# Kernel tuning notes

Measured on AMD Instinct MI355X. Metric: run time of the kernel, lower is better.

## Reference

```python
import jax, jax.numpy as jnp
import numpy as np

B = 4096
HIST = 50
VOCAB = 100000
PAD_IDX = 179
EMB_DIM = 64           # sparse_dim_after_embedding
DENSE = 256            # dense_feature_number
PROJ_IN = 768          # emb_feature_dim_before_project
PROJ_HID = 256
PROJ_OUT = 64          # emb_feature_dim
BOT = (512, 64)        # bottom_mlp_dims
ALL_DIM = EMB_DIM + BOT[1] + PROJ_OUT        # 192
OUT_DIM = ALL_DIM * (ALL_DIM + 1) // 2 + BOT[1]  # 18592
TOP = (1024, 512)      # top_mlp_dims
BN_EPS = 1e-5

# precomputed upper-triangular (incl. diagonal) indices, row-major like torch mask extract
_TRIU_R, _TRIU_C = np.triu_indices(ALL_DIM)


def setup_inputs() -> dict:
    key = jax.random.key(0)
    ks = jax.random.split(key, 20)
    s = 0.02
    emb_table = jax.random.normal(ks[0], (VOCAB, EMB_DIM), jnp.float32) * s
    emb_table = emb_table.at[PAD_IDX].set(0.0)  # padding_idx=179
    return {
        "x_sparse": jax.random.randint(ks[1], (B, HIST), 0, VOCAB),
        "x_dense": jax.random.normal(ks[2], (B, DENSE), jnp.float32),
        "x_embed_before_projection": jax.random.normal(ks[3], (B, PROJ_IN), jnp.float32),
        "emb_table": emb_table,
        "pw1": jax.random.normal(ks[4], (PROJ_IN, PROJ_HID), jnp.float32) * s,
        "pb1": jnp.zeros((PROJ_HID,), jnp.float32),
        "pw2": jax.random.normal(ks[5], (PROJ_HID, PROJ_OUT), jnp.float32) * s,
        "pb2": jnp.zeros((PROJ_OUT,), jnp.float32),
        "bn_gamma": jnp.ones((PROJ_OUT,), jnp.float32),
        "bn_beta": jnp.zeros((PROJ_OUT,), jnp.float32),
        "bw1": jax.random.normal(ks[6], (DENSE, BOT[0]), jnp.float32) * s,
        "bb1": jnp.zeros((BOT[0],), jnp.float32),
        "bw2": jax.random.normal(ks[7], (BOT[0], BOT[1]), jnp.float32) * s,
        "bb2": jnp.zeros((BOT[1],), jnp.float32),
        "tw1": jax.random.normal(ks[8], (OUT_DIM, TOP[0]), jnp.float32) * s,
        "tb1": jnp.zeros((TOP[0],), jnp.float32),
        "tw2": jax.random.normal(ks[9], (TOP[0], TOP[1]), jnp.float32) * s,
        "tb2": jnp.zeros((TOP[1],), jnp.float32),
        "tw3": jax.random.normal(ks[10], (TOP[1], 1), jnp.float32) * s,
        "tb3": jnp.zeros((1,), jnp.float32),
    }


def reference(x_sparse, x_dense, x_embed_before_projection, emb_table,
              pw1, pb1, pw2, pb2, bn_gamma, bn_beta,
              bw1, bb1, bw2, bb2, tw1, tb1, tw2, tb2, tw3, tb3):
    # embedding-sum over history: [B, HIST, EMB_DIM] -> [B, EMB_DIM]
    embed_x = jnp.sum(emb_table[x_sparse], axis=1)

    # ContrastiveNet: Linear -> ReLU -> Linear -> BatchNorm1d (batch stats, training fwd)
    h = jax.nn.relu(x_embed_before_projection @ pw1 + pb1)
    z = h @ pw2 + pb2
    mu = jnp.mean(z, axis=0)
    var = jnp.var(z, axis=0)  # biased variance, as torch BN uses for normalization
    x_embed = bn_gamma * (z - mu) * jax.lax.rsqrt(var + BN_EPS) + bn_beta

    # bottom MLP (dropout = identity at inference)
    bottom = jax.nn.relu(jax.nn.relu(x_dense @ bw1 + bb1) @ bw2 + bb2)

    concat_first = jnp.concatenate([bottom, x_embed, embed_x], axis=-1)  # [B, 192]

    # pairwise dot-product interaction; pack upper triangle incl. diagonal
    dot = jnp.einsum('bi,bj->bij', concat_first, concat_first)  # [B, 192, 192]
    interaction = dot[:, _TRIU_R, _TRIU_C]  # [B, 192*193/2]

    concat_second = jnp.concatenate([interaction, bottom], axis=-1)  # [B, OUT_DIM]

    t = jax.nn.relu(concat_second @ tw1 + tb1)
    t = jax.nn.relu(t @ tw2 + tb2)
    output = jax.nn.sigmoid(t @ tw3 + tb3)  # [B, 1]
    # squeeze(-1).squeeze().unsqueeze(1) -> [B, 1]
    output = output.reshape(-1, 1)
    return output, x_embed
```

## Files before the change

### kernel.cpp

```cpp
#include <hip/hip_runtime.h>
#include <hip/hip_bf16.h>
#include <cstdint>
#include <cstddef>

typedef __bf16 bf16;
typedef unsigned char u8;
typedef unsigned short u16;
typedef __bf16 v8bf  __attribute__((ext_vector_type(8)));
typedef float  f32x4 __attribute__((ext_vector_type(4)));
typedef float  f32x16 __attribute__((ext_vector_type(16)));
typedef int    i32x4 __attribute__((ext_vector_type(4)));
typedef int    i32x2 __attribute__((ext_vector_type(2)));
typedef int    v8i32 __attribute__((ext_vector_type(8)));

__device__ __forceinline__ void async16(void* lds, const void* g) {
  __builtin_amdgcn_global_load_lds(
      (const __attribute__((address_space(1))) unsigned int*)g,
      (__attribute__((address_space(3))) unsigned int*)lds, 16, 0, 0);
}


__device__ __forceinline__ void pairs_dev(u16* __restrict__ pairs, float* __restrict__ stats) {
  int r = threadIdx.x;
  if (r < 128) stats[r] = 0.f;
  if (r < 192) {
    int off = 192 * r - (r * (r - 1)) / 2;
    for (int c = r; c < 192; ++c) pairs[off + c - r] = (u16)((r << 8) | c);
  } else if (r == 192) {
    for (int j = 0; j < 64; ++j) pairs[18528 + j] = (u16)((j << 8) | 192);
  } else if (r == 193) {
    for (int j = 18592; j < 18624; ++j) pairs[j] = (u16)((192 << 8) | 192);
  }
}

__device__ __forceinline__ void packA_dev(const float* __restrict__ A,
                                          bf16* __restrict__ Ap, int K,
                                          int bx, int by) {
  const int t = threadIdx.x;
  const int KT = K >> 5;
  const size_t tile = ((size_t)bx * KT + by) * (64 * 32);
  const int c = t;
  const int mm = c >> 2, koct = (c & 3) * 8;
  const float* src = A + (size_t)(bx * 64 + mm) * K + by * 32 + koct;
  f32x4 f0 = *(const f32x4*)src;
  f32x4 f1 = *(const f32x4*)(src + 4);
  __align__(16) bf16 h[8];
  h[0]=(bf16)f0[0]; h[1]=(bf16)f0[1]; h[2]=(bf16)f0[2]; h[3]=(bf16)f0[3];
  h[4]=(bf16)f1[0]; h[5]=(bf16)f1[1]; h[6]=(bf16)f1[2]; h[7]=(bf16)f1[3];
  *(i32x4*)(Ap + tile + (size_t)c * 8) = *(const i32x4*)h;
}

__device__ __forceinline__ void packB_dev(const float* __restrict__ B,
                                          bf16* __restrict__ Bp, int K, int N,
                                          int bx, int by,
                                          float* __restrict__ sLB) {
  const int BNp = 64, LS = 66;
  const int t = threadIdx.x;
  const int KT = K >> 5;
  for (int idx = t; idx < 32 * BNp; idx += 256) {
    const int kk = idx >> 6, nn = idx & 63;
    sLB[kk * LS + nn] = B[(size_t)(by * 32 + kk) * N + bx * BNp + nn];
  }
  __syncthreads();
  const size_t tile = ((size_t)bx * KT + by) * ((size_t)BNp * 32);
  for (int c = t; c < BNp * 4; c += 256) {
    const int nn = c >> 2, koct = (c & 3) * 8;
    __align__(16) bf16 h[8];
#pragma unroll
    for (int j = 0; j < 8; ++j) h[j] = (bf16)sLB[(koct + j) * LS + nn];
    *(i32x4*)(Bp + tile + (size_t)c * 8) = *(const i32x4*)h;
  }
}

__device__ __forceinline__ void packTw1_dev(const float* __restrict__ tw1,
                                            u8* __restrict__ Bp, int nt, int kw) {
  const int t = threadIdx.x;
  const int n4 = t & 31, k8 = t >> 5;
  const int kbase = kw * 64 + k8 * 8;
  const int nbase = nt * 128 + n4 * 4;
  f32x4 v[8];
#pragma unroll
  for (int j = 0; j < 8; ++j) {
    const int gk = kbase + j;
    if (gk < 18592) {
      v[j] = *(const f32x4*)(tw1 + (size_t)gk * 1024 + nbase);
      v[j] *= 32.f;
    } else {
      v[j] = f32x4{0.f, 0.f, 0.f, 0.f};
    }
  }
  u8* tile = Bp + ((size_t)nt * 291 + kw) * 8192;
#pragma unroll
  for (int c = 0; c < 4; ++c) {
    int r0 = __builtin_amdgcn_cvt_pk_fp8_f32(v[0][c], v[1][c], 0, false);
    r0 = __builtin_amdgcn_cvt_pk_fp8_f32(v[2][c], v[3][c], r0, true);
    int r1 = __builtin_amdgcn_cvt_pk_fp8_f32(v[4][c], v[5][c], 0, false);
    r1 = __builtin_amdgcn_cvt_pk_fp8_f32(v[6][c], v[7][c], r1, true);
    i32x2 d; d[0] = r0; d[1] = r1;
    *(i32x2*)(tile + (n4 * 4 + c) * 64 + k8 * 8) = d;
  }
}

__global__ __launch_bounds__(256) void prologue_kernel(
    const float* __restrict__ xep, const float* __restrict__ xd,
    const float* __restrict__ pw1, const float* __restrict__ pw2,
    const float* __restrict__ bw1, const float* __restrict__ bw2,
    const float* __restrict__ tw1, const float* __restrict__ tw2,
    bf16* Xp, bf16* Xd, bf16* Bpw1, bf16* Bpw2, bf16* Bbw1, bf16* Bbw2,
    u8* Btw1, bf16* Btw2, u16* pairs, float* stats) {
  __shared__ float sLB[32 * 66];
  int i = blockIdx.x;
  if (i < 2328) { packTw1_dev(tw1, Btw1, i & 7, i >> 3); return; }
  i -= 2328;
  if (i < 1536) { packA_dev(xep, Xp, 768, i & 63, i >> 6); return; }
  i -= 1536;
  if (i < 512)  { packA_dev(xd, Xd, 256, i & 63, i >> 6); return; }
  i -= 512;
  if (i < 96)   { packB_dev(pw1, Bpw1, 768, 256, i & 3, i >> 2, sLB); return; }
  i -= 96;
  if (i < 8)    { packB_dev(pw2, Bpw2, 256, 64, 0, i, sLB); return; }
  i -= 8;
  if (i < 64)   { packB_dev(bw1, Bbw1, 256, 512, i & 7, i >> 3, sLB); return; }
  i -= 64;
  if (i < 16)   { packB_dev(bw2, Bbw2, 512, 64, 0, i, sLB); return; }
  i -= 16;
  if (i < 256)  { packB_dev(tw2, Btw2, 1024, 512, i & 7, i >> 3, sLB); return; }
  i -= 256;
  if (i == 0) pairs_dev(pairs, stats);
}

__device__ __forceinline__ void embed8_dev(const int* __restrict__ xs,
                                           const float* __restrict__ emb,
                                           float* __restrict__ cf, int blk) {
  const int wid = threadIdx.x >> 6, lane = threadIdx.x & 63;
#pragma unroll
  for (int s = 0; s < 2; ++s) {
    const int b = blk * 8 + s * 4 + wid;
    const int* row = xs + (size_t)b * 50;
    float acc = 0.f;
#pragma unroll 10
    for (int h = 0; h < 50; ++h) {
      int idx = row[h];
      acc += emb[(size_t)idx * 64 + lane];
    }
    cf[(size_t)b * 193 + 128 + lane] = acc;
  }
}

template <int BM, int BN, int MF, int NF>
__device__ __forceinline__ void gemm_body(
    const bf16* __restrict__ Ap, const bf16* __restrict__ Bp,
    const float* __restrict__ bias,
    float* __restrict__ outF, int ldF,
    bf16* __restrict__ outP, int ktN, int bmsh,
    int KT, int M0, int relu_flag, int bx, int by,
    bf16* sA, bf16* sB, float* statsAcc) {
  const int t = threadIdx.x;
  const int wid = t >> 6, lane = t & 63;
  const int wm = (wid >> 1) * (MF * 16);
  const int wn = (wid & 1) * (NF * 16);
  const int r16 = lane & 15, q = lane >> 4;

  f32x4 acc[MF][NF];
#pragma unroll
  for (int i = 0; i < MF; ++i)
#pragma unroll
    for (int j = 0; j < NF; ++j) acc[i][j] = f32x4{0.f, 0.f, 0.f, 0.f};

  const bf16* aBase = Ap + (size_t)bx * KT * (BM * 32);
  const bf16* bBase = Bp + (size_t)by * KT * (BN * 32);
  constexpr int A_CH = BM * 4;
  constexpr int B_CH = BN * 4;

  for (int kt = 0; kt < KT; ++kt) {
    const bf16* ag = aBase + (size_t)kt * (BM * 32);
    const bf16* bg = bBase + (size_t)kt * (BN * 32);
#pragma unroll
    for (int c = t; c < A_CH; c += 256) {
      const int row = c >> 2, qs = c & 3, qg = (qs - (row >> 1)) & 3;
      async16(sA + c * 8, ag + row * 32 + qg * 8);
    }
#pragma unroll
    for (int c = t; c < B_CH; c += 256) {
      const int row = c >> 2, qs = c & 3, qg = (qs - (row >> 1)) & 3;
      async16(sB + c * 8, bg + row * 32 + qg * 8);
    }
    __syncthreads();
    v8bf af[MF], bfr[NF];
#pragma unroll
    for (int i = 0; i < MF; ++i) {
      const int row = wm + i * 16 + r16;
      af[i] = *(const v8bf*)(sA + row * 32 + (((q + (row >> 1)) & 3) * 8));
    }
#pragma unroll
    for (int j = 0; j < NF; ++j) {
      const int row = wn + j * 16 + r16;
      bfr[j] = *(const v8bf*)(sB + row * 32 + (((q + (row >> 1)) & 3) * 8));
    }
#pragma unroll
    for (int i = 0; i < MF; ++i)
#pragma unroll
      for (int j = 0; j < NF; ++j)
        acc[i][j] = __builtin_amdgcn_mfma_f32_16x16x32_bf16(af[i], bfr[j], acc[i][j], 0, 0, 0);
    __syncthreads();
  }

  float cs[NF], cs2[NF];
#pragma unroll
  for (int j = 0; j < NF; ++j) { cs[j] = 0.f; cs2[j] = 0.f; }

#pragma unroll
  for (int j = 0; j < NF; ++j) {
    const int gn = by * BN + wn + j * 16 + r16;
    const float bv = bias[gn];
#pragma unroll
    for (int i = 0; i < MF; ++i) {
      const int gm0 = M0 + bx * BM + wm + i * 16 + q * 4;
#pragma unroll
      for (int r = 0; r < 4; ++r) {
        float v = acc[i][j][r] + bv;
        if (relu_flag) v = fmaxf(v, 0.f);
        if (statsAcc) { cs[j] += v; cs2[j] += v * v; }
        const int gm = gm0 + r;
        if (outF) outF[(size_t)gm * ldF + gn] = v;
        if (outP) {
          const int mt = gm >> bmsh, mm = gm & ((1 << bmsh) - 1);
          outP[(((size_t)mt * ktN + (gn >> 5)) << (bmsh + 5)) + ((size_t)mm << 5) + (gn & 31)] = (bf16)v;
        }
      }
    }
  }

  if (statsAcc) {
#pragma unroll
    for (int j = 0; j < NF; ++j) {
      float a = cs[j], b2 = cs2[j];
      a += __shfl_xor(a, 16, 64);  a += __shfl_xor(a, 32, 64);
      b2 += __shfl_xor(b2, 16, 64); b2 += __shfl_xor(b2, 32, 64);
      if (q == 0) {
        const int gn = by * BN + wn + j * 16 + r16;
        atomicAdd(&statsAcc[gn], a);
        atomicAdd(&statsAcc[64 + gn], b2);
      }
    }
  }
}

template <int BM, int BN, int MF, int NF>
__global__ __launch_bounds__(256, 2) void gemm_kernel(
    const bf16* __restrict__ Ap, const bf16* __restrict__ Bp,
    const float* __restrict__ bias,
    float* __restrict__ outF, int ldF,
    bf16* __restrict__ outP, int ktN, int bmsh,
    int KT, int M0, int relu_flag) {
  __shared__ __align__(16) bf16 sA[BM * 32];
  __shared__ __align__(16) bf16 sB[BN * 32];
  gemm_body<BM, BN, MF, NF>(Ap, Bp, bias, outF, ldF, outP, ktN, bmsh,
                            KT, M0, relu_flag, blockIdx.x, blockIdx.y, sA, sB, nullptr);
}

template <int BM, int BN, int MF, int NF>
__global__ __launch_bounds__(256, 2) void gemm_dual_kernel(
    const bf16* Ap0, const bf16* Bp0, const float* bias0,
    float* outF0, int ldF0, bf16* outP0, int ktN0, int bmsh0, int KT0, int relu0, int gy0,
    float* statsAcc0,
    const bf16* Ap1, const bf16* Bp1, const float* bias1,
    float* outF1, int ldF1, bf16* outP1, int ktN1, int bmsh1, int KT1, int relu1, int gy1,
    const int* xs, const float* emb, float* cf) {
  __shared__ __align__(16) bf16 sA[BM * 32];
  __shared__ __align__(16) bf16 sB[BN * 32];
  if (blockIdx.z == 0) {
    if ((int)blockIdx.y >= gy0) return;
    gemm_body<BM, BN, MF, NF>(Ap0, Bp0, bias0, outF0, ldF0, outP0, ktN0, bmsh0,
                              KT0, 0, relu0, blockIdx.x, blockIdx.y, sA, sB, statsAcc0);
  } else if (blockIdx.z == 1) {
    if ((int)blockIdx.y >= gy1) return;
    gemm_body<BM, BN, MF, NF>(Ap1, Bp1, bias1, outF1, ldF1, outP1, ktN1, bmsh1,
                              KT1, 0, relu1, blockIdx.x, blockIdx.y, sA, sB, nullptr);
  } else {
    embed8_dev(xs, emb, cf, blockIdx.y * 64 + blockIdx.x);
  }
}

template <int S>
__global__ __launch_bounds__(256, 4) void gemm_splitk_mx(
    const u8* __restrict__ Ap, const u8* __restrict__ Bp,
    bf16* __restrict__ part, int Mchunk) {
  __shared__ __align__(16) u8 sAB[4][8192];
  const int t = threadIdx.x;
  const int bx = blockIdx.x, by = blockIdx.y, bz = blockIdx.z;
  const int lane = t & 63, wid = t >> 6;
  const int wm = (wid >> 1) * 64, wn = (wid & 1) * 64;
  const int l31 = lane & 31, khalf = lane >> 5;
  const int kw0 = (291 * bz) / S, kw1 = (291 * (bz + 1)) / S;

  const int r1 = t >> 2;
  const int g1 = r1 * 64 + ((((t & 3) - (r1 >> 1)) & 3) << 4);
  const int r2 = (t + 256) >> 2;
  const int g2 = r2 * 64 + (((((t + 256) & 3) - (r2 >> 1)) & 3) << 4);
  u8* lA = &sAB[0][0] + t * 16;
  u8* lB = &sAB[2][0] + t * 16;

  const u8* fa0[2]; const u8* fa1[2]; const u8* fb0[2]; const u8* fb1[2];
#pragma unroll
  for (int i = 0; i < 2; ++i) {
    const int ra = wm + i * 32 + l31;
    const int qa = (khalf * 2 + (ra >> 1)) & 3;
    fa0[i] = &sAB[0][0] + ra * 64 + qa * 16;
    fa1[i] = &sAB[0][0] + ra * 64 + (((qa + 1) & 3) << 4);
    const int rb = wn + i * 32 + l31;
    const int qb = (khalf * 2 + (rb >> 1)) & 3;
    fb0[i] = &sAB[2][0] + rb * 64 + qb * 16;
    fb1[i] = &sAB[2][0] + rb * 64 + (((qb + 1) & 3) << 4);
  }

  f32x16 acc[2][2];
#pragma unroll
  for (int i = 0; i < 2; ++i)
#pragma unroll
    for (int j = 0; j < 2; ++j)
#pragma unroll
      for (int r = 0; r < 16; ++r) acc[i][j][r] = 0.f;

  const u8* agp = Ap + ((size_t)bx * 291 + kw0) * 8192;
  const u8* bgp = Bp + ((size_t)by * 291 + kw0) * 8192;

  auto compute = [&](int off) {
    v8i32 av[2], bv[2];
#pragma unroll
    for (int i = 0; i < 2; ++i) {
      union { i32x4 h[2]; v8i32 v; } ua;
      ua.h[0] = *(const i32x4*)(fa0[i] + off);
      ua.h[1] = *(const i32x4*)(fa1[i] + off);
      av[i] = ua.v;
      union { i32x4 h[2]; v8i32 v; } ub;
      ub.h[0] = *(const i32x4*)(fb0[i] + off);
      ub.h[1] = *(const i32x4*)(fb1[i] + off);
      bv[i] = ub.v;
    }
#pragma unroll
    for (int i = 0; i < 2; ++i)
#pragma unroll
      for (int j = 0; j < 2; ++j)
        acc[i][j] = __builtin_amdgcn_mfma_scale_f32_32x32x64_f8f6f4(
            av[i], bv[j], acc[i][j], 0, 0,
            0, 0x7F7F7F7F,
            0, 0x7A7A7A7A);
  };

  const int nw = kw1 - kw0;

  async16(lA, agp + g1);  async16(lA + 4096, agp + g2);
  async16(lB, bgp + g1);  async16(lB + 4096, bgp + g2);

  for (int w = 0; w < nw; ++w) {
    const int cur = (w & 1) * 8192;
    const int nxt = 8192 - cur;
    if (w + 1 < nw) {
      const u8* ag = agp + (size_t)(w + 1) * 8192;
      const u8* bg = bgp + (size_t)(w + 1) * 8192;
      async16(lA + nxt, ag + g1);  async16(lA + nxt + 4096, ag + g2);
      async16(lB + nxt, bg + g1);  async16(lB + nxt + 4096, bg + g2);
      asm volatile("s_waitcnt vmcnt(4)" ::: "memory");
    } else {
      asm volatile("s_waitcnt vmcnt(0)" ::: "memory");
    }
    __builtin_amdgcn_s_barrier();
    __builtin_amdgcn_sched_barrier(0);
    __builtin_amdgcn_s_setprio(1);
    compute(cur);
    __builtin_amdgcn_s_setprio(0);
    __builtin_amdgcn_s_barrier();
  }

  bf16* pBase = part + (size_t)bz * Mchunk * 1024;
#pragma unroll
  for (int i = 0; i < 2; ++i)
#pragma unroll
    for (int j = 0; j < 2; ++j) {
      const int gn = by * 128 + wn + j * 32 + l31;
#pragma unroll
      for (int r = 0; r < 16; ++r) {
        const int gm = bx * 128 + wm + i * 32 + (r & 3) + 8 * (r >> 2) + 4 * khalf;
        pBase[(size_t)gm * 1024 + gn] = (bf16)acc[i][j][r];
      }
    }
}

__global__ __launch_bounds__(256) void reducek_kernel(const bf16* __restrict__ part,
                                                      const float* __restrict__ bias,
                                                      bf16* __restrict__ t1,
                                                      int S, int Mchunk, int M0) {
  const int idx = blockIdx.x * 256 + threadIdx.x;
  const int gm = idx >> 7;
  const int gn8 = (idx & 127) * 8;
  float v[8] = {0.f, 0.f, 0.f, 0.f, 0.f, 0.f, 0.f, 0.f};
  for (int s = 0; s < S; ++s) {
    v8bf p = *(const v8bf*)(part + ((size_t)s * Mchunk + gm) * 1024 + gn8);
#pragma unroll
    for (int r = 0; r < 8; ++r) v[r] += (float)p[r];
  }
  const f32x4 b0 = *(const f32x4*)(bias + gn8);
  const f32x4 b1 = *(const f32x4*)(bias + gn8 + 4);
  __align__(16) bf16 h[8];
#pragma unroll
  for (int r = 0; r < 4; ++r) h[r] = (bf16)fmaxf(v[r] + b0[r], 0.f);
#pragma unroll
  for (int r = 0; r < 4; ++r) h[4 + r] = (bf16)fmaxf(v[4 + r] + b1[r], 0.f);
  const int G = M0 + gm;
  const int mt = G >> 6, mm = G & 63, kt = gn8 >> 5;
  *(i32x4*)(t1 + (((size_t)mt * 32 + kt) << 11) + (mm << 5) + (gn8 & 31)) = *(const i32x4*)h;
}

__global__ __launch_bounds__(256, 2) void agen_kernel(const float* __restrict__ cf,
                                                      const float* __restrict__ z,
                                                      const float* __restrict__ gsum,
                                                      const float* __restrict__ gamma,
                                                      const float* __restrict__ beta,
                                                      const u16* __restrict__ pairs,
                                                      u8* __restrict__ Ap,
                                                      float* __restrict__ dout,
                                                      int rowBase) {
  __shared__ float sCF[64 * 193];
  __shared__ float sMu[64], sRstd[64];
  const int t = threadIdx.x;
  const int gRow0 = rowBase + blockIdx.x * 64;
  for (int idx = t; idx < 64 * 64; idx += 256) {
    const int r = idx >> 6, c = idx & 63;
    sCF[r * 193 + c] = cf[(size_t)(gRow0 + r) * 193 + c];
  }
  for (int idx = t; idx < 64 * 64; idx += 256) {
    const int r = idx >> 6, c = idx & 63;
    sCF[r * 193 + 128 + c] = cf[(size_t)(gRow0 + r) * 193 + 128 + c];
  }
  if (t < 64) {
    const float mu = gsum[t] * (1.f / 4096.f);
    const float var = gsum[64 + t] * (1.f / 4096.f) - mu * mu;
    sMu[t] = mu;
    sRstd[t] = rsqrtf(var + 1e-5f);
    sCF[t * 193 + 192] = 1.f;
  }
  __syncthreads();
  for (int idx = t; idx < 64 * 64; idx += 256) {
    const int r = idx >> 6, c = idx & 63;
    const float xe = gamma[c] * (z[(size_t)(gRow0 + r) * 64 + c] - sMu[c]) * sRstd[c] + beta[c];
    sCF[r * 193 + 64 + c] = xe;
    if (blockIdx.y == 0) dout[4096 + (size_t)(gRow0 + r) * 64 + c] = xe;
  }
  __syncthreads();

  const int kw0 = (291 * blockIdx.y) / 8;
  const int kw1 = (291 * (blockIdx.y + 1)) / 8;
  const int row = t >> 2, kq = t & 3;
  const int mt = blockIdx.x >> 1;
  const int mrow = (blockIdx.x & 1) * 64 + row;
  const float* myrow = sCF + row * 193;
  for (int kw = kw0; kw < kw1; ++kw) {
    const int kb = kw * 64 + kq * 16;
    i32x4 d;
    if (kb >= 18592) {
      d = i32x4{0, 0, 0, 0};
    } else {
      union { i32x4 v4[2]; u16 u[16]; } P;
      P.v4[0] = *(const i32x4*)(pairs + kb);
      P.v4[1] = *(const i32x4*)(pairs + kb + 8);
#pragma unroll
      for (int g = 0; g < 4; ++g) {
        float p[4];
#pragma unroll
        for (int j = 0; j < 4; ++j) {
          const u16 pr = P.u[g * 4 + j];
          p[j] = myrow[pr >> 8] * myrow[pr & 255];
        }
        int r = __builtin_amdgcn_cvt_pk_fp8_f32(p[0], p[1], 0, false);
        r = __builtin_amdgcn_cvt_pk_fp8_f32(p[2], p[3], r, true);
        d[g] = r;
      }
    }
    *(i32x4*)(Ap + (((size_t)mt * 291 + kw) * 128 + mrow) * 64 + kq * 16) = d;
  }
}

__global__ __launch_bounds__(256) void topdot_kernel(const bf16* __restrict__ t2p,
                                                     const float* __restrict__ w,
                                                     const float* __restrict__ b3,
                                                     float* __restrict__ dout) {
  const int wid = threadIdx.x >> 6, lane = threadIdx.x & 63;
  const int b = blockIdx.x * 4 + wid;
  const size_t addr = ((((size_t)(b >> 6) * 16) + (lane >> 2)) << 11) +
                      ((size_t)(b & 63) << 5) + (lane & 3) * 8;
  v8bf p = *(const v8bf*)(t2p + addr);
  const float* wv = w + lane * 8;
  float s = 0.f;
#pragma unroll
  for (int r = 0; r < 8; ++r) s += (float)p[r] * wv[r];
  for (int m = 32; m > 0; m >>= 1) s += __shfl_xor(s, m, 64);
  if (lane == 0) dout[b] = 1.f / (1.f + __expf(-(s + b3[0])));
}

extern "C" void kernel_launch(void* const* d_in, const int* in_sizes, int n_in,
                              void* d_out, int out_size, void* d_ws, size_t ws_size,
                              hipStream_t stream) {
  const int*   xs   = (const int*)  d_in[0];
  const float* xd   = (const float*)d_in[1];
  const float* xep  = (const float*)d_in[2];
  const float* emb  = (const float*)d_in[3];
  const float* pw1  = (const float*)d_in[4];
  const float* pb1  = (const float*)d_in[5];
  const float* pw2  = (const float*)d_in[6];
  const float* pb2  = (const float*)d_in[7];
  const float* gmma = (const float*)d_in[8];
  const float* beta = (const float*)d_in[9];
  const float* bw1  = (const float*)d_in[10];
  const float* bb1  = (const float*)d_in[11];
  const float* bw2  = (const float*)d_in[12];
  const float* bb2  = (const float*)d_in[13];
  const float* tw1  = (const float*)d_in[14];
  const float* tb1  = (const float*)d_in[15];
  const float* tw2  = (const float*)d_in[16];
  const float* tb2  = (const float*)d_in[17];
  const float* tw3  = (const float*)d_in[18];
  const float* tb3  = (const float*)d_in[19];
  float* out = (float*)d_out;

  uint8_t* base = (uint8_t*)d_ws;
  size_t off = 0;
  auto alloc = [&](size_t b) {
    void* p = base + off;
    off = (off + b + 511) & ~((size_t)511);
    return p;
  };
  u16*  pairs = (u16*) alloc((size_t)18624 * 2);
  bf16* Xp    = (bf16*)alloc((size_t)4096 * 768 * 2);
  bf16* Xd    = (bf16*)alloc((size_t)4096 * 256 * 2);
  bf16* Bpw1  = (bf16*)alloc((size_t)768 * 256 * 2);
  bf16* Bpw2  = (bf16*)alloc((size_t)256 * 64 * 2);
  bf16* Bbw1  = (bf16*)alloc((size_t)256 * 512 * 2);
  bf16* Bbw2  = (bf16*)alloc((size_t)512 * 64 * 2);
  u8*   Btw1  = (u8*)  alloc((size_t)8 * 291 * 8192);
  bf16* Btw2  = (bf16*)alloc((size_t)1024 * 512 * 2);
  bf16* hbuf  = (bf16*)alloc((size_t)4096 * 256 * 2);
  float* z    = (float*)alloc((size_t)4096 * 64 * 4);
  float* stats= (float*)alloc((size_t)128 * 4);
  bf16* b0    = (bf16*)alloc((size_t)4096 * 512 * 2);
  float* cf   = (float*)alloc((size_t)4096 * 193 * 4);
  bf16* t1    = (bf16*)alloc((size_t)4096 * 1024 * 2);
  bf16* t2p   = (bf16*)alloc((size_t)4096 * 512 * 2);
  size_t fixedEnd = off;

  int chunk = 512, S = 8;
  {
    const int candC[5] = {4096, 2048, 2048, 1024, 512};
    const int candS[5] = {4, 8, 4, 8, 8};
    for (int i = 0; i < 5; ++i) {
      size_t need = fixedEnd + (size_t)candC[i] * 18624 + 1024 +
                    (size_t)candS[i] * candC[i] * 1024 * 2 + 1024;
      if (need <= ws_size) { chunk = candC[i]; S = candS[i]; break; }
    }
  }
  u8*   ApBig = (u8*)  alloc((size_t)chunk * 18624);
  bf16* partK = (bf16*)alloc((size_t)S * chunk * 1024 * 2);

  prologue_kernel<<<4817, 256, 0, stream>>>(
      xep, xd, pw1, pw2, bw1, bw2, tw1, tw2,
      Xp, Xd, Bpw1, Bpw2, Bbw1, Bbw2, Btw1, Btw2, pairs, stats);

  gemm_dual_kernel<64, 64, 2, 2><<<dim3(64, 8, 3), 256, 0, stream>>>(
      Xp, Bpw1, pb1, nullptr, 0, hbuf, 8, 6, 24, 1, 4, nullptr,
      Xd, Bbw1, bb1, nullptr, 0, b0, 16, 6, 8, 1, 8,
      xs, emb, cf);
  gemm_dual_kernel<64, 64, 2, 2><<<dim3(64, 1, 2), 256, 0, stream>>>(
      hbuf, Bpw2, pb2, z, 64, nullptr, 0, 0, 8, 0, 1, stats,
      b0, Bbw2, bb2, cf, 193, nullptr, 0, 0, 16, 1, 1,
      nullptr, nullptr, nullptr);

  for (int c0 = 0; c0 < 4096; c0 += chunk) {
    agen_kernel<<<dim3(chunk / 64, 8), 256, 0, stream>>>(
        cf, z, stats, gmma, beta, pairs, ApBig, out, c0);
    if (S == 4)
      gemm_splitk_mx<4><<<dim3(chunk / 128, 8, 4), 256, 0, stream>>>(
          ApBig, Btw1, partK, chunk);
    else
      gemm_splitk_mx<8><<<dim3(chunk / 128, 8, 8), 256, 0, stream>>>(
          ApBig, Btw1, partK, chunk);
    reducek_kernel<<<chunk / 2, 256, 0, stream>>>(partK, tb1, t1, S, chunk, c0);
  }

  gemm_kernel<64, 64, 2, 2><<<dim3(64, 8), 256, 0, stream>>>(
      t1, Btw2, tb2, nullptr, 0, t2p, 16, 6, 32, 0, 1);
  topdot_kernel<<<1024, 256, 0, stream>>>(t2p, tw3, tb3, out);
}
```

Baseline: 354.0 us.

## Stage two K-tiles per barrier in split-K MX GEMM with larger LDS buffers

The split-K FP8 MFMA GEMM now loads pairs of K-tiles into a doubled 64KB LDS double buffer, so each barrier round covers two tiles of compute. This halves the number of barrier synchronisations and gives each prefetch more time to land. The setprio calls are dropped and launch bounds fall from 4 to 2 waves per SIMD to fit the larger LDS footprint, which lowers occupancy.

```diff
diff --git a/kernel.cpp b/kernel.cpp
--- a/kernel.cpp
+++ b/kernel.cpp
@@ -283,35 +283,37 @@
 }
 
 template <int S>
-__global__ __launch_bounds__(256, 4) void gemm_splitk_mx(
+__global__ __launch_bounds__(256, 2) void gemm_splitk_mx(
     const u8* __restrict__ Ap, const u8* __restrict__ Bp,
     bf16* __restrict__ part, int Mchunk) {
-  __shared__ __align__(16) u8 sAB[4][8192];
+  __shared__ __align__(16) u8 sAB[65536];
   const int t = threadIdx.x;
   const int bx = blockIdx.x, by = blockIdx.y, bz = blockIdx.z;
   const int lane = t & 63, wid = t >> 6;
   const int wm = (wid >> 1) * 64, wn = (wid & 1) * 64;
   const int l31 = lane & 31, khalf = lane >> 5;
   const int kw0 = (291 * bz) / S, kw1 = (291 * (bz + 1)) / S;
+  const int nw = kw1 - kw0;
+  const int np = (nw + 1) >> 1;
 
   const int r1 = t >> 2;
   const int g1 = r1 * 64 + ((((t & 3) - (r1 >> 1)) & 3) << 4);
   const int r2 = (t + 256) >> 2;
   const int g2 = r2 * 64 + (((((t + 256) & 3) - (r2 >> 1)) & 3) << 4);
-  u8* lA = &sAB[0][0] + t * 16;
-  u8* lB = &sAB[2][0] + t * 16;
+  u8* lA = &sAB[0] + t * 16;
+  u8* lB = &sAB[32768] + t * 16;
 
   const u8* fa0[2]; const u8* fa1[2]; const u8* fb0[2]; const u8* fb1[2];
 #pragma unroll
   for (int i = 0; i < 2; ++i) {
     const int ra = wm + i * 32 + l31;
     const int qa = (khalf * 2 + (ra >> 1)) & 3;
-    fa0[i] = &sAB[0][0] + ra * 64 + qa * 16;
-    fa1[i] = &sAB[0][0] + ra * 64 + (((qa + 1) & 3) << 4);
+    fa0[i] = &sAB[0] + ra * 64 + qa * 16;
+    fa1[i] = &sAB[0] + ra * 64 + (((qa + 1) & 3) << 4);
     const int rb = wn + i * 32 + l31;
     const int qb = (khalf * 2 + (rb >> 1)) & 3;
-    fb0[i] = &sAB[2][0] + rb * 64 + qb * 16;
-    fb1[i] = &sAB[2][0] + rb * 64 + (((qb + 1) & 3) << 4);
+    fb0[i] = &sAB[32768] + rb * 64 + qb * 16;
+    fb1[i] = &sAB[32768] + rb * 64 + (((qb + 1) & 3) << 4);
   }
 
   f32x16 acc[2][2];
@@ -324,6 +326,20 @@
 
   const u8* agp = Ap + ((size_t)bx * 291 + kw0) * 8192;
   const u8* bgp = Bp + ((size_t)by * 291 + kw0) * 8192;
+
+  auto stagePair = [&](int p) {
+    const int w0 = p * 2;
+    const int w1 = (p * 2 + 1 < nw) ? p * 2 + 1 : nw - 1;
+    const int dst = (p & 1) * 16384;
+    const u8* ag0 = agp + (size_t)w0 * 8192;
+    const u8* ag1 = agp + (size_t)w1 * 8192;
+    const u8* bg0 = bgp + (size_t)w0 * 8192;
+    const u8* bg1 = bgp + (size_t)w1 * 8192;
+    async16(lA + dst, ag0 + g1);         async16(lA + dst + 4096, ag0 + g2);
+    async16(lA + dst + 8192, ag1 + g1);  async16(lA + dst + 12288, ag1 + g2);
+    async16(lB + dst, bg0 + g1);         async16(lB + dst + 4096, bg0 + g2);
+    async16(lB + dst + 8192, bg1 + g1);  async16(lB + dst + 12288, bg1 + g2);
+  };
 
   auto compute = [&](int off) {
     v8i32 av[2], bv[2];
@@ -348,29 +364,24 @@
             0, 0x7A7A7A7A);
   };
 
-  const int nw = kw1 - kw0;
-
-  async16(lA, agp + g1);  async16(lA + 4096, agp + g2);
-  async16(lB, bgp + g1);  async16(lB + 4096, bgp + g2);
-
-  for (int w = 0; w < nw; ++w) {
-    const int cur = (w & 1) * 8192;
-    const int nxt = 8192 - cur;
-    if (w + 1 < nw) {
-      const u8* ag = agp + (size_t)(w + 1) * 8192;
-      const u8* bg = bgp + (size_t)(w + 1) * 8192;
-      async16(lA + nxt, ag + g1);  async16(lA + nxt + 4096, ag + g2);
-      async16(lB + nxt, bg + g1);  async16(lB + nxt + 4096, bg + g2);
-      asm volatile("s_waitcnt vmcnt(4)" ::: "memory");
+  stagePair(0);
+  for (int p = 0; p < np; ++p) {
+    const bool more = (p + 1 < np);
+    if (more) {
+      stagePair(p + 1);
+      asm volatile("s_waitcnt vmcnt(8)" ::: "memory");
     } else {
       asm volatile("s_waitcnt vmcnt(0)" ::: "memory");
     }
     __builtin_amdgcn_s_barrier();
     __builtin_amdgcn_sched_barrier(0);
-    __builtin_amdgcn_s_setprio(1);
-    compute(cur);
-    __builtin_amdgcn_s_setprio(0);
-    __builtin_amdgcn_s_barrier();
+    const int off = (p & 1) * 16384;
+    compute(off);
+    if (p * 2 + 1 < nw) compute(off + 8192);
+    if (more) {
+      asm volatile("s_waitcnt lgkmcnt(0)" ::: "memory");
+      __builtin_amdgcn_s_barrier();
+    }
   }
 
   bf16* pBase = part + (size_t)bz * Mchunk * 1024;
```

After: 350.1 us. Within noise of the previous version (-1.1%).

## Enlarge split-K MX-FP8 GEMM tile to 256x128 per block

Applied to the files above, without the earlier changes.

The top-MLP split-K FP8 GEMM block now covers 256 rows of M instead of 128, with each wave computing a 128x64 sub-tile (4x2 MFMAs). Each B fragment loaded from LDS is reused across twice as many MFMAs, and the grid is halved. LDS grows to 48KB and accumulator registers double, so launch bounds drop to 2 blocks per CU. The setprio calls are removed and the trailing barrier is skipped on the last iteration. Fewer blocks per chunk may hurt load balance and latency hiding.

```diff
diff --git a/kernel.cpp b/kernel.cpp
--- a/kernel.cpp
+++ b/kernel.cpp
@@ -283,105 +283,122 @@
 }
 
 template <int S>
-__global__ __launch_bounds__(256, 4) void gemm_splitk_mx(
+__global__ __launch_bounds__(256, 2) void gemm_splitk_mx(
     const u8* __restrict__ Ap, const u8* __restrict__ Bp,
     bf16* __restrict__ part, int Mchunk) {
-  __shared__ __align__(16) u8 sAB[4][8192];
+  __shared__ __align__(16) u8 sAB[49152];
   const int t = threadIdx.x;
   const int bx = blockIdx.x, by = blockIdx.y, bz = blockIdx.z;
   const int lane = t & 63, wid = t >> 6;
-  const int wm = (wid >> 1) * 64, wn = (wid & 1) * 64;
+  const int wm2 = (wid >> 1) * 128, wn = (wid & 1) * 64;
   const int l31 = lane & 31, khalf = lane >> 5;
   const int kw0 = (291 * bz) / S, kw1 = (291 * (bz + 1)) / S;
-
-  const int r1 = t >> 2;
-  const int g1 = r1 * 64 + ((((t & 3) - (r1 >> 1)) & 3) << 4);
-  const int r2 = (t + 256) >> 2;
-  const int g2 = r2 * 64 + (((((t + 256) & 3) - (r2 >> 1)) & 3) << 4);
-  u8* lA = &sAB[0][0] + t * 16;
-  u8* lB = &sAB[2][0] + t * 16;
-
-  const u8* fa0[2]; const u8* fa1[2]; const u8* fb0[2]; const u8* fb1[2];
-#pragma unroll
-  for (int i = 0; i < 2; ++i) {
-    const int ra = wm + i * 32 + l31;
+  const int nw = kw1 - kw0;
+
+  const size_t TILE1 = (size_t)291 * 8192;
+  size_t aSrc[4]; int aDst[4];
+#pragma unroll
+  for (int k = 0; k < 4; ++k) {
+    const int c = t + 256 * k;
+    const int ra = c >> 2;
+    const int qg = ((c & 3) - (ra >> 1)) & 3;
+    aSrc[k] = (ra >= 128 ? TILE1 + (size_t)(ra - 128) * 64 : (size_t)ra * 64) + qg * 16;
+    aDst[k] = t * 16 + k * 4096;
+  }
+  size_t bSrc[2]; int bDst[2];
+#pragma unroll
+  for (int k = 0; k < 2; ++k) {
+    const int c = t + 256 * k;
+    const int rb = c >> 2;
+    const int qg = ((c & 3) - (rb >> 1)) & 3;
+    bSrc[k] = (size_t)rb * 64 + qg * 16;
+    bDst[k] = 16384 + t * 16 + k * 4096;
+  }
+
+  int fa0[4], fa1[4], fb0[2], fb1[2];
+#pragma unroll
+  for (int i = 0; i < 4; ++i) {
+    const int ra = wm2 + i * 32 + l31;
     const int qa = (khalf * 2 + (ra >> 1)) & 3;
-    fa0[i] = &sAB[0][0] + ra * 64 + qa * 16;
-    fa1[i] = &sAB[0][0] + ra * 64 + (((qa + 1) & 3) << 4);
-    const int rb = wn + i * 32 + l31;
+    fa0[i] = ra * 64 + qa * 16;
+    fa1[i] = ra * 64 + (((qa + 1) & 3) << 4);
+  }
+#pragma unroll
+  for (int j = 0; j < 2; ++j) {
+    const int rb = wn + j * 32 + l31;
     const int qb = (khalf * 2 + (rb >> 1)) & 3;
-    fb0[i] = &sAB[2][0] + rb * 64 + qb * 16;
-    fb1[i] = &sAB[2][0] + rb * 64 + (((qb + 1) & 3) << 4);
-  }
-
-  f32x16 acc[2][2];
-#pragma unroll
-  for (int i = 0; i < 2; ++i)
+    fb0[j] = 16384 + rb * 64 + qb * 16;
+    fb1[j] = 16384 + rb * 64 + (((qb + 1) & 3) << 4);
+  }
+
+  f32x16 acc[4][2];
+#pragma unroll
+  for (int i = 0; i < 4; ++i)
 #pragma unroll
     for (int j = 0; j < 2; ++j)
 #pragma unroll
       for (int r = 0; r < 16; ++r) acc[i][j][r] = 0.f;
 
-  const u8* agp = Ap + ((size_t)bx * 291 + kw0) * 8192;
+  const u8* agp = Ap + ((size_t)(bx * 2) * 291 + kw0) * 8192;
   const u8* bgp = Bp + ((size_t)by * 291 + kw0) * 8192;
 
+  auto stageW = [&](int w) {
+    const int slot = (w & 1) * 24576;
+    const u8* ag = agp + (size_t)w * 8192;
+    const u8* bg = bgp + (size_t)w * 8192;
+#pragma unroll
+    for (int k = 0; k < 4; ++k) async16(&sAB[slot + aDst[k]], ag + aSrc[k]);
+#pragma unroll
+    for (int k = 0; k < 2; ++k) async16(&sAB[slot + bDst[k]], bg + bSrc[k]);
+  };
+
   auto compute = [&](int off) {
-    v8i32 av[2], bv[2];
-#pragma unroll
-    for (int i = 0; i < 2; ++i) {
+    v8i32 bv[2];
+#pragma unroll
+    for (int j = 0; j < 2; ++j) {
+      union { i32x4 h[2]; v8i32 v; } ub;
+      ub.h[0] = *(const i32x4*)&sAB[fb0[j] + off];
+      ub.h[1] = *(const i32x4*)&sAB[fb1[j] + off];
+      bv[j] = ub.v;
+    }
+#pragma unroll
+    for (int i = 0; i < 4; ++i) {
       union { i32x4 h[2]; v8i32 v; } ua;
-      ua.h[0] = *(const i32x4*)(fa0[i] + off);
-      ua.h[1] = *(const i32x4*)(fa1[i] + off);
-      av[i] = ua.v;
-      union { i32x4 h[2]; v8i32 v; } ub;
-      ub.h[0] = *(const i32x4*)(fb0[i] + off);
-      ub.h[1] = *(const i32x4*)(fb1[i] + off);
-      bv[i] = ub.v;
-    }
-#pragma unroll
-    for (int i = 0; i < 2; ++i)
-#pragma unroll
-      for (int j = 0; j < 2; ++j)
-        acc[i][j] = __builtin_amdgcn_mfma_scale_f32_32x32x64_f8f6f4(
-            av[i], bv[j], acc[i][j], 0, 0,
-            0, 0x7F7F7F7F,
-            0, 0x7A7A7A7A);
+      ua.h[0] = *(const i32x4*)&sAB[fa0[i] + off];
+      ua.h[1] = *(const i32x4*)&sAB[fa1[i] + off];
+      acc[i][0] = __builtin_amdgcn_mfma_scale_f32_32x32x64_f8f6f4(
+          ua.v, bv[0], acc[i][0], 0, 0, 0, 0x7F7F7F7F, 0, 0x7A7A7A7A);
+      acc[i][1] = __builtin_amdgcn_mfma_scale_f32_32x32x64_f8f6f4(
+          ua.v, bv[1], acc[i][1], 0, 0, 0, 0x7F7F7F7F, 0, 0x7A7A7A7A);
+    }
   };
 
-  const int nw = kw1 - kw0;
-
-  async16(lA, agp + g1);  async16(lA + 4096, agp + g2);
-  async16(lB, bgp + g1);  async16(lB + 4096, bgp + g2);
-
+  stageW(0);
   for (int w = 0; w < nw; ++w) {
-    const int cur = (w & 1) * 8192;
-    const int nxt = 8192 - cur;
     if (w + 1 < nw) {
-      const u8* ag = agp + (size_t)(w + 1) * 8192;
-      const u8* bg = bgp + (size_t)(w + 1) * 8192;
-      async16(lA + nxt, ag + g1);  async16(lA + nxt + 4096, ag + g2);
-      async16(lB + nxt, bg + g1);  async16(lB + nxt + 4096, bg + g2);
-      asm volatile("s_waitcnt vmcnt(4)" ::: "memory");
+      stageW(w + 1);
+      asm volatile("s_waitcnt vmcnt(6)" ::: "memory");
     } else {
       asm volatile("s_waitcnt vmcnt(0)" ::: "memory");
     }
     __builtin_amdgcn_s_barrier();
     __builtin_amdgcn_sched_barrier(0);
-    __builtin_amdgcn_s_setprio(1);
-    compute(cur);
-    __builtin_amdgcn_s_setprio(0);
-    __builtin_amdgcn_s_barrier();
+    compute((w & 1) * 24576);
+    if (w + 1 < nw) {
+      asm volatile("s_waitcnt lgkmcnt(0)" ::: "memory");
+      __builtin_amdgcn_s_barrier();
+    }
   }
 
   bf16* pBase = part + (size_t)bz * Mchunk * 1024;
 #pragma unroll
-  for (int i = 0; i < 2; ++i)
+  for (int i = 0; i < 4; ++i)
 #pragma unroll
     for (int j = 0; j < 2; ++j) {
       const int gn = by * 128 + wn + j * 32 + l31;
 #pragma unroll
       for (int r = 0; r < 16; ++r) {
-        const int gm = bx * 128 + wm + i * 32 + (r & 3) + 8 * (r >> 2) + 4 * khalf;
+        const int gm = bx * 256 + wm2 + i * 32 + (r & 3) + 8 * (r >> 2) + 4 * khalf;
         pBase[(size_t)gm * 1024 + gn] = (bf16)acc[i][j][r];
       }
     }
@@ -578,10 +595,10 @@
     agen_kernel<<<dim3(chunk / 64, 8), 256, 0, stream>>>(
         cf, z, stats, gmma, beta, pairs, ApBig, out, c0);
     if (S == 4)
-      gemm_splitk_mx<4><<<dim3(chunk / 128, 8, 4), 256, 0, stream>>>(
+      gemm_splitk_mx<4><<<dim3(chunk / 256, 8, 4), 256, 0, stream>>>(
           ApBig, Btw1, partK, chunk);
     else
-      gemm_splitk_mx<8><<<dim3(chunk / 128, 8, 8), 256, 0, stream>>>(
+      gemm_splitk_mx<8><<<dim3(chunk / 256, 8, 8), 256, 0, stream>>>(
           ApBig, Btw1, partK, chunk);
     reducek_kernel<<<chunk / 2, 256, 0, stream>>>(partK, tb1, t1, S, chunk, c0);
   }
```

Result: faster. 342.9 us, median of 2 (-3.1%).
